# Performance work log

Measured on AMD Instinct MI355X. Metric: run time of the kernel, lower is better.

The kernel has to match this reference:

```python
import jax, jax.numpy as jnp
import numpy as np

N = 50000
E = 800000
IN_DIM, HID, OUT = 128, 256, 40
BN_EPS = 1e-5


def setup_inputs() -> dict:
    key = jax.random.key(0)
    ks = jax.random.split(key, 10)
    x = jax.random.normal(ks[0], (N, IN_DIM), dtype=jnp.float32)
    edge_index = jax.random.randint(ks[1], (2, E), 0, N, dtype=jnp.int64)
    W1 = jax.random.normal(ks[2], (IN_DIM, HID), dtype=jnp.float32) * 0.05
    b1 = jnp.zeros((HID,), dtype=jnp.float32)
    W2 = jax.random.normal(ks[3], (HID, HID), dtype=jnp.float32) * 0.05
    b2 = jnp.zeros((HID,), dtype=jnp.float32)
    W3 = jax.random.normal(ks[4], (HID, OUT), dtype=jnp.float32) * 0.05
    b3 = jnp.zeros((OUT,), dtype=jnp.float32)
    # BatchNorm params (shared across the two pre-final layers in the source)
    gamma = jnp.ones((HID,), dtype=jnp.float32)
    beta = jnp.zeros((HID,), dtype=jnp.float32)
    return {"x": x, "edge_index": edge_index, "W1": W1, "b1": b1,
            "W2": W2, "b2": b2, "W3": W3, "b3": b3,
            "gamma": gamma, "beta": beta}


def _gcn_norm(edge_index):
    # add self-loops, compute symmetric normalization D^-1/2 (A+I) D^-1/2
    self_loops = jnp.arange(N, dtype=edge_index.dtype)
    row = jnp.concatenate([edge_index[0], self_loops])
    col = jnp.concatenate([edge_index[1], self_loops])
    deg = jax.ops.segment_sum(jnp.ones_like(row, dtype=jnp.float32), col, num_segments=N)
    dinv = jnp.where(deg > 0, jax.lax.rsqrt(deg), 0.0)
    norm = dinv[row] * dinv[col]  # [E+N]
    return row, col, norm


def _gcn_conv(h, W, b, row, col, norm):
    h = h @ W                              # transform first (smaller msg dim)
    msg = norm[:, None] * h[col]           # [E+N, F] gather
    agg = jax.ops.segment_sum(msg, row, num_segments=N)  # scatter-add
    return agg + b


def _batchnorm(h, gamma, beta):
    mu = jnp.mean(h, axis=0)
    var = jnp.mean((h - mu) ** 2, axis=0)
    return (h - mu) * jax.lax.rsqrt(var + BN_EPS) * gamma + beta


def reference(x, edge_index, W1, b1, W2, b2, W3, b3, gamma, beta):
    row, col, norm = _gcn_norm(edge_index)
    out = _gcn_conv(x, W1, b1, row, col, norm)
    out = jax.nn.relu(_batchnorm(out, gamma, beta))
    out = _gcn_conv(out, W2, b2, row, col, norm)
    out = jax.nn.relu(_batchnorm(out, gamma, beta))  # BN shared in source
    out = _gcn_conv(out, W3, b3, row, col, norm)
    return jax.nn.log_softmax(out, axis=-1)
```

## Files before the change

kernel.cpp:

```cpp
#include <hip/hip_runtime.h>
#include <math.h>

#define NN 50000
#define NE 800000
#define IN_DIM 128
#define HID 256
#define OUT_DIM 40
#define BN_EPS 1e-5f

#define HG 128
#define HW 25000
#define HPASS 12800

#define NBK 196
#define PB 256
#define EPB (NE / PB)

typedef __attribute__((ext_vector_type(8))) short short8;
typedef __attribute__((ext_vector_type(4))) float f32x4;
typedef __attribute__((ext_vector_type(2))) float f32x2;

__device__ __forceinline__ ushort f2bf(float f) {
    union { float f; unsigned u; } v; v.f = f;
    unsigned r = v.u + 0x7fffu + ((v.u >> 16) & 1u);
    return (ushort)(r >> 16);
}
__device__ __forceinline__ float bflo(unsigned u) {
    union { unsigned a; float f; } v; v.a = u << 16; return v.f;
}
__device__ __forceinline__ float bfhi(unsigned u) {
    union { unsigned a; float f; } v; v.a = u & 0xffff0000u; return v.f;
}
__device__ __forceinline__ f32x2 fp8_dec_lo(int v) {
    return __builtin_amdgcn_cvt_pk_f32_fp8(v, false);
}
__device__ __forceinline__ f32x2 fp8_dec_hi(int v) {
    return __builtin_amdgcn_cvt_pk_f32_fp8(v, true);
}
__device__ __forceinline__ int fp8_enc_lo(float a, float b, int old) {
    return __builtin_amdgcn_cvt_pk_fp8_f32(a, b, old, false);
}
__device__ __forceinline__ int fp8_enc_hi(float a, float b, int old) {
    return __builtin_amdgcn_cvt_pk_fp8_f32(a, b, old, true);
}

__global__ __launch_bounds__(512) void k_p1(const int* __restrict__ erow,
                                            const int* __restrict__ ecol,
                                            unsigned* __restrict__ Pcol,
                                            unsigned* __restrict__ cnt) {
    __shared__ unsigned lds[HPASS];
    int t = threadIdx.x;
    int b = blockIdx.x;
    if (b < HG) {
        unsigned* partial = Pcol + (size_t)b * HW;
        int e0 = b * (NE / HG), e1 = e0 + (NE / HG);
#pragma unroll
        for (int pass = 0; pass < 2; pass++) {
            int wbase = pass ? HPASS : 0;
            int wend = pass ? HW : HPASS;
            int nw = wend - wbase;
            for (int w = t; w < HPASS; w += 512) lds[w] = 0u;
            __syncthreads();
            int vlo = wbase * 2, vhi = wend * 2;
            for (int e = e0 + t; e < e1; e += 512) {
                int v = ecol[e];
                if (v >= vlo && v < vhi)
                    atomicAdd(&lds[(v >> 1) - wbase], (v & 1) ? 0x10000u : 1u);
            }
            __syncthreads();
            for (int w = t; w < nw; w += 512) partial[wbase + w] = lds[w];
            __syncthreads();
        }
    } else {
        int bb = b - HG;
        for (int i = t; i < NBK; i += 512) lds[i] = 0u;
        __syncthreads();
        int e0 = bb * EPB;
        for (int i = t; i < EPB; i += 512) atomicAdd(&lds[((unsigned)erow[e0 + i]) >> 8], 1u);
        __syncthreads();
        for (int i = t; i < NBK; i += 512) cnt[bb * NBK + i] = lds[i];
    }
}

__global__ __launch_bounds__(256) void k_p2(const unsigned* __restrict__ Pcol,
                                            float* __restrict__ dinv,
                                            const unsigned* __restrict__ cnt,
                                            unsigned* __restrict__ off,
                                            unsigned* __restrict__ bstart) {
    int t = threadIdx.x;
    if (blockIdx.x < 98) {
        int w = blockIdx.x * 256 + t;
        if (w >= HW) return;
        unsigned sc = 0;
        for (int b = 0; b < HG; b++) sc += Pcol[(size_t)b * HW + w];
        dinv[2 * w] = rsqrtf((float)((sc & 0xffffu) + 1u));
        dinv[2 * w + 1] = rsqrtf((float)((sc >> 16) + 1u));
    } else {
        __shared__ unsigned s[256];
        unsigned tot = 0;
        if (t < NBK) for (int b = 0; b < PB; b++) tot += cnt[b * NBK + t];
        s[t] = tot;
        __syncthreads();
        for (int o = 1; o < 256; o <<= 1) {
            unsigned x = (t >= o) ? s[t - o] : 0u;
            __syncthreads();
            s[t] += x;
            __syncthreads();
        }
        unsigned base = s[t] - tot;
        if (t < NBK) bstart[t] = base;
        if (t == NBK - 1) bstart[NBK] = base + tot;
        if (t < NBK) {
            unsigned run = base;
            for (int b = 0; b < PB; b++) { off[b * NBK + t] = run; run += cnt[b * NBK + t]; }
        }
    }
}

__global__ __launch_bounds__(256) void k_p3(const int* __restrict__ erow,
                                            const int* __restrict__ ecol,
                                            const unsigned* __restrict__ off,
                                            int2* __restrict__ ebuf,
                                            const float* __restrict__ x,
                                            const float* __restrict__ dinv,
                                            uchar* __restrict__ xs8,
                                            const float* __restrict__ W1,
                                            const float* __restrict__ W2,
                                            const float* __restrict__ W3,
                                            ushort* __restrict__ Wt1,
                                            ushort* __restrict__ Wt2,
                                            ushort* __restrict__ Wt3) {
    int t = threadIdx.x, b = blockIdx.x;
    if (b < PB) {
        __shared__ unsigned c[NBK];
        for (int i = t; i < NBK; i += 256) c[i] = off[b * NBK + i];
        __syncthreads();
        int e0 = b * EPB;
        for (int i = t; i < EPB; i += 256) {
            int r = erow[e0 + i], cc = ecol[e0 + i];
            unsigned p = atomicAdd(&c[((unsigned)r) >> 8], 1u);
            ebuf[p] = make_int2(r, cc);
        }
    } else if (b < PB + 6250) {
        int i = (b - PB) * 256 + t;
        int row = i >> 5;
        float d = dinv[row];
        float4 v = ((const float4*)x)[i];
        int p = fp8_enc_lo(v.x * d, v.y * d, 0);
        p = fp8_enc_hi(v.z * d, v.w * d, p);
        ((int*)xs8)[i] = p;
    } else {
        int i = (b - PB - 6250) * 256 + t;
        if (i < 128 * 256) { int k = i / 256, n = i % 256; Wt1[n * 128 + k] = f2bf(W1[i]); }
        if (i < 256 * 256) { int k = i / 256, n = i % 256; Wt2[n * 256 + k] = f2bf(W2[i]); }
        if (i < 48 * 256)  { int n = i / 256, k = i % 256;
                             Wt3[i] = (n < OUT_DIM) ? f2bf(W3[k * OUT_DIM + n]) : (ushort)0; }
    }
}

__global__ __launch_bounds__(256) void k_part4(const int2* __restrict__ ebuf,
                                               const unsigned* __restrict__ bstart,
                                               unsigned* __restrict__ rowptr,
                                               int* __restrict__ colidx) {
    __shared__ unsigned rc[256], cur[256], s[256];
    int t = threadIdx.x, b = blockIdx.x;
    unsigned ebase = bstart[b], ecnt = bstart[b + 1] - ebase;
    rc[t] = 0u;
    __syncthreads();
    for (unsigned i = t; i < ecnt; i += 256) atomicAdd(&rc[ebuf[ebase + i].x & 255], 1u);
    __syncthreads();
    unsigned v = rc[t];
    s[t] = v;
    __syncthreads();
    for (int o = 1; o < 256; o <<= 1) {
        unsigned x = (t >= o) ? s[t - o] : 0u;
        __syncthreads();
        s[t] += x;
        __syncthreads();
    }
    unsigned excl = s[t] - v;
    int row = (b << 8) + t;
    if (row < NN) rowptr[row] = ebase + excl;
    cur[t] = ebase + excl;
    if (b == 0 && t == 0) rowptr[NN] = NE;
    __syncthreads();
    for (unsigned i = t; i < ecnt; i += 256) {
        int2 e = ebuf[ebase + i];
        unsigned p = atomicAdd(&cur[e.x & 255], 1u);
        colidx[p] = e.y;
    }
}

__global__ __launch_bounds__(64) void k_agg_x(const uchar* __restrict__ xs8,
                                              const unsigned* __restrict__ rowptr,
                                              const int* __restrict__ colidx,
                                              const float* __restrict__ dinv,
                                              ushort* __restrict__ Xa) {
    int r = blockIdx.x;
    int t = threadIdx.x;
    const ushort* Xv = (const ushort*)xs8;
    f32x2 sf = fp8_dec_lo((int)Xv[(size_t)r * 64 + t]);
    float a0 = sf[0], a1 = sf[1];
    unsigned e0 = rowptr[r], e1 = rowptr[r + 1];
    unsigned e = e0;
    for (; e + 8 <= e1; e += 8) {
        int v0 = Xv[(size_t)colidx[e] * 64 + t];
        int v1 = Xv[(size_t)colidx[e + 1] * 64 + t];
        int v2 = Xv[(size_t)colidx[e + 2] * 64 + t];
        int v3 = Xv[(size_t)colidx[e + 3] * 64 + t];
        int v4 = Xv[(size_t)colidx[e + 4] * 64 + t];
        int v5 = Xv[(size_t)colidx[e + 5] * 64 + t];
        int v6 = Xv[(size_t)colidx[e + 6] * 64 + t];
        int v7 = Xv[(size_t)colidx[e + 7] * 64 + t];
        f32x2 f0 = fp8_dec_lo(v0), f1 = fp8_dec_lo(v1);
        f32x2 f2 = fp8_dec_lo(v2), f3 = fp8_dec_lo(v3);
        f32x2 f4 = fp8_dec_lo(v4), f5 = fp8_dec_lo(v5);
        f32x2 f6 = fp8_dec_lo(v6), f7 = fp8_dec_lo(v7);
        a0 += f0[0] + f1[0] + f2[0] + f3[0] + f4[0] + f5[0] + f6[0] + f7[0];
        a1 += f0[1] + f1[1] + f2[1] + f3[1] + f4[1] + f5[1] + f6[1] + f7[1];
    }
    for (; e < e1; e++) {
        f32x2 f = fp8_dec_lo((int)Xv[(size_t)colidx[e] * 64 + t]);
        a0 += f[0]; a1 += f[1];
    }
    float dr = dinv[r];
    ((unsigned*)Xa)[(size_t)r * 64 + t] = (unsigned)f2bf(dr * a0) | ((unsigned)f2bf(dr * a1) << 16);
}

template <int K>
__global__ __launch_bounds__(256) void k_gemm1(const ushort* __restrict__ A,
                                               const ushort* __restrict__ Bt,
                                               ushort* __restrict__ H16,
                                               float* __restrict__ bnacc) {
    constexpr int BK = 32;
    constexpr int LD = 40;
    __shared__ ushort sA[64 * LD];
    __shared__ ushort sB[128 * LD];
    int t = threadIdx.x;
    int wave = t >> 6, lane = t & 63;
    int quad = lane >> 4, m15 = lane & 15;
    long r0 = (long)blockIdx.x * 64;
    int n0 = blockIdx.y * 128;

    f32x4 acc[8];
#pragma unroll
    for (int i = 0; i < 8; i++) { acc[i][0] = 0.f; acc[i][1] = 0.f; acc[i][2] = 0.f; acc[i][3] = 0.f; }

    for (int k0 = 0; k0 < K; k0 += BK) {
        {
            int row = t >> 2, seg = (t & 3) * 8;
            long gr = r0 + row;
            uint4 v = make_uint4(0, 0, 0, 0);
            if (gr < NN) v = *(const uint4*)(A + gr * K + k0 + seg);
            *(uint4*)(sA + row * LD + seg) = v;
        }
        {
            int n = t >> 1, seg = (t & 1) * 16;
            const uint4* src = (const uint4*)(Bt + (long)(n0 + n) * K + k0 + seg);
            uint4 b0 = src[0], b1 = src[1];
            *(uint4*)(sB + n * LD + seg) = b0;
            *(uint4*)(sB + n * LD + seg + 8) = b1;
        }
        __syncthreads();
        short8 a = *(const short8*)(sA + (wave * 16 + m15) * LD + quad * 8);
#pragma unroll
        for (int ct = 0; ct < 8; ct++) {
            short8 b = *(const short8*)(sB + (ct * 16 + m15) * LD + quad * 8);
            acc[ct] = __builtin_amdgcn_mfma_f32_16x16x32_bf16(a, b, acc[ct], 0, 0, 0);
        }
        __syncthreads();
    }
    long rowbase = r0 + wave * 16 + quad * 4;
#pragma unroll
    for (int ct = 0; ct < 8; ct++) {
        int col = n0 + ct * 16 + m15;
#pragma unroll
        for (int rg = 0; rg < 4; rg++) {
            long gr = rowbase + rg;
            if (gr < NN) H16[gr * 256 + col] = f2bf(acc[ct][rg]);
        }
    }
    float* ldsS = (float*)(void*)sA;
    float* ldsQ = (float*)(void*)sB;
#pragma unroll
    for (int ct = 0; ct < 8; ct++) {
        float s = acc[ct][0] + acc[ct][1] + acc[ct][2] + acc[ct][3];
        float q = acc[ct][0] * acc[ct][0] + acc[ct][1] * acc[ct][1]
                + acc[ct][2] * acc[ct][2] + acc[ct][3] * acc[ct][3];
        s += __shfl_xor(s, 16, 64); q += __shfl_xor(q, 16, 64);
        s += __shfl_xor(s, 32, 64); q += __shfl_xor(q, 32, 64);
        if (quad == 0) {
            ldsS[wave * 128 + ct * 16 + m15] = s;
            ldsQ[wave * 128 + ct * 16 + m15] = q;
        }
    }
    __syncthreads();
    {
        int c = t & 127;
        int slice = blockIdx.x & 7;
        float v = (t < 128)
            ? ldsS[c] + ldsS[128 + c] + ldsS[256 + c] + ldsS[384 + c]
            : ldsQ[c] + ldsQ[128 + c] + ldsQ[256 + c] + ldsQ[384 + c];
        atomicAdd(&bnacc[slice * 512 + ((t < 128) ? 0 : 256) + n0 + c], v);
    }
}

__device__ __forceinline__ void bn_stage8(const ushort* __restrict__ Hrow, bool valid,
                                          const float* __restrict__ bn, int col0,
                                          ushort* __restrict__ dst) {
    uint4 hv = make_uint4(0, 0, 0, 0);
    if (valid) hv = *(const uint4*)(Hrow + col0);
    float f[8] = { bflo(hv.x), bfhi(hv.x), bflo(hv.y), bfhi(hv.y),
                   bflo(hv.z), bfhi(hv.z), bflo(hv.w), bfhi(hv.w) };
#pragma unroll
    for (int j = 0; j < 8; j++)
        dst[j] = f2bf(fmaxf(f[j] * bn[512 + col0 + j] + bn[768 + col0 + j], 0.f));
}

__global__ __launch_bounds__(256) void k_gemm2(const ushort* __restrict__ H16,
                                               const float* __restrict__ bn,
                                               const ushort* __restrict__ Bt,
                                               const float* __restrict__ dinv,
                                               uchar* __restrict__ Y8) {
    constexpr int K = 256, BK = 32, LD = 40;
    __shared__ ushort sA[64 * LD];
    __shared__ ushort sB[128 * LD];
    int t = threadIdx.x;
    int wave = t >> 6, lane = t & 63;
    int quad = lane >> 4, m15 = lane & 15;
    long r0 = (long)blockIdx.x * 64;
    int n0 = blockIdx.y * 128;

    f32x4 acc[8];
#pragma unroll
    for (int i = 0; i < 8; i++) { acc[i][0] = 0.f; acc[i][1] = 0.f; acc[i][2] = 0.f; acc[i][3] = 0.f; }

    for (int k0 = 0; k0 < K; k0 += BK) {
        {
            int row = t >> 2, seg = (t & 3) * 8;
            long gr = r0 + row;
            bn_stage8(H16 + gr * 256, gr < NN, bn, k0 + seg, sA + row * LD + seg);
        }
        {
            int n = t >> 1, seg = (t & 1) * 16;
            const uint4* src = (const uint4*)(Bt + (long)(n0 + n) * K + k0 + seg);
            uint4 b0 = src[0], b1 = src[1];
            *(uint4*)(sB + n * LD + seg) = b0;
            *(uint4*)(sB + n * LD + seg + 8) = b1;
        }
        __syncthreads();
        short8 a = *(const short8*)(sA + (wave * 16 + m15) * LD + quad * 8);
#pragma unroll
        for (int ct = 0; ct < 8; ct++) {
            short8 b = *(const short8*)(sB + (ct * 16 + m15) * LD + quad * 8);
            acc[ct] = __builtin_amdgcn_mfma_f32_16x16x32_bf16(a, b, acc[ct], 0, 0, 0);
        }
        __syncthreads();
    }
    long rowbase = r0 + wave * 16 + quad * 4;
    float dv[4];
#pragma unroll
    for (int rg = 0; rg < 4; rg++) dv[rg] = (rowbase + rg < NN) ? dinv[rowbase + rg] : 0.f;
#pragma unroll
    for (int ct = 0; ct < 8; ct++) {
        int col = n0 + ct * 16 + m15;
#pragma unroll
        for (int rg = 0; rg < 4; rg++) {
            long gr = rowbase + rg;
            if (gr < NN) {
                int p = fp8_enc_lo(dv[rg] * acc[ct][rg], 0.f, 0);
                Y8[gr * 256 + col] = (uchar)(p & 0xff);
            }
        }
    }
}

__global__ __launch_bounds__(256) void k_gemm3(const ushort* __restrict__ H16,
                                               const float* __restrict__ bn,
                                               const ushort* __restrict__ Wt3,
                                               const float* __restrict__ dinv,
                                               ushort* __restrict__ Y) {
    constexpr int LD = 264;
    __shared__ ushort sA[64 * LD];
    __shared__ ushort sB[48 * LD];
    int t = threadIdx.x;
    int wave = t >> 6, lane = t & 63;
    int quad = lane >> 4, m15 = lane & 15;
    long r0 = (long)blockIdx.x * 64;

    for (int idx = t; idx < 48 * 16; idx += 256) {
        int n = idx >> 4, s = (idx & 15) * 16;
        const uint4* src = (const uint4*)(Wt3 + n * 256 + s);
        *(uint4*)(sB + n * LD + s) = src[0];
        *(uint4*)(sB + n * LD + s + 8) = src[1];
    }
    {
        int row = t >> 2;
        long gr = r0 + row;
#pragma unroll
        for (int s8 = 0; s8 < 8; s8++) {
            int seg = s8 * 32 + (t & 3) * 8;
            bn_stage8(H16 + gr * 256, gr < NN, bn, seg, sA + row * LD + seg);
        }
    }
    __syncthreads();

    f32x4 acc[3];
#pragma unroll
    for (int i = 0; i < 3; i++) { acc[i][0] = 0.f; acc[i][1] = 0.f; acc[i][2] = 0.f; acc[i][3] = 0.f; }
#pragma unroll
    for (int k0 = 0; k0 < 256; k0 += 32) {
        short8 a = *(const short8*)(sA + (wave * 16 + m15) * LD + k0 + quad * 8);
#pragma unroll
        for (int ct = 0; ct < 3; ct++) {
            short8 b = *(const short8*)(sB + (ct * 16 + m15) * LD + k0 + quad * 8);
            acc[ct] = __builtin_amdgcn_mfma_f32_16x16x32_bf16(a, b, acc[ct], 0, 0, 0);
        }
    }
    long rowbase = r0 + wave * 16 + quad * 4;
#pragma unroll
    for (int ct = 0; ct < 3; ct++) {
        int col = ct * 16 + m15;
#pragma unroll
        for (int rg = 0; rg < 4; rg++) {
            long gr = rowbase + rg;
            if (gr < NN) Y[gr * 64 + col] = f2bf(dinv[gr] * acc[ct][rg]);
        }
    }
}

__global__ __launch_bounds__(64) void k_agg_hid(const uchar* __restrict__ Y8,
                                                const unsigned* __restrict__ rowptr,
                                                const int* __restrict__ colidx,
                                                const float* __restrict__ dinv,
                                                ushort* __restrict__ H16) {
    int r = blockIdx.x;
    int t = threadIdx.x;
    const int* Yv = (const int*)Y8;
    int y = Yv[(size_t)r * 64 + t];
    f32x2 yl = fp8_dec_lo(y), yh = fp8_dec_hi(y);
    float a0 = yl[0], a1 = yl[1], a2 = yh[0], a3 = yh[1];
    unsigned e0 = rowptr[r], e1 = rowptr[r + 1];
    unsigned e = e0;
    for (; e + 8 <= e1; e += 8) {
        int v0 = Yv[(size_t)colidx[e] * 64 + t];
        int v1 = Yv[(size_t)colidx[e + 1] * 64 + t];
        int v2 = Yv[(size_t)colidx[e + 2] * 64 + t];
        int v3 = Yv[(size_t)colidx[e + 3] * 64 + t];
        int v4 = Yv[(size_t)colidx[e + 4] * 64 + t];
        int v5 = Yv[(size_t)colidx[e + 5] * 64 + t];
        int v6 = Yv[(size_t)colidx[e + 6] * 64 + t];
        int v7 = Yv[(size_t)colidx[e + 7] * 64 + t];
        f32x2 l0 = fp8_dec_lo(v0), h0 = fp8_dec_hi(v0);
        f32x2 l1 = fp8_dec_lo(v1), h1 = fp8_dec_hi(v1);
        f32x2 l2 = fp8_dec_lo(v2), h2 = fp8_dec_hi(v2);
        f32x2 l3 = fp8_dec_lo(v3), h3 = fp8_dec_hi(v3);
        f32x2 l4 = fp8_dec_lo(v4), h4 = fp8_dec_hi(v4);
        f32x2 l5 = fp8_dec_lo(v5), h5 = fp8_dec_hi(v5);
        f32x2 l6 = fp8_dec_lo(v6), h6 = fp8_dec_hi(v6);
        f32x2 l7 = fp8_dec_lo(v7), h7 = fp8_dec_hi(v7);
        a0 += l0[0] + l1[0] + l2[0] + l3[0] + l4[0] + l5[0] + l6[0] + l7[0];
        a1 += l0[1] + l1[1] + l2[1] + l3[1] + l4[1] + l5[1] + l6[1] + l7[1];
        a2 += h0[0] + h1[0] + h2[0] + h3[0] + h4[0] + h5[0] + h6[0] + h7[0];
        a3 += h0[1] + h1[1] + h2[1] + h3[1] + h4[1] + h5[1] + h6[1] + h7[1];
    }
    for (; e < e1; e++) {
        int v = Yv[(size_t)colidx[e] * 64 + t];
        f32x2 l = fp8_dec_lo(v), h = fp8_dec_hi(v);
        a0 += l[0]; a1 += l[1]; a2 += h[0]; a3 += h[1];
    }
    float dr = dinv[r];
    uint2 o;
    o.x = (unsigned)f2bf(dr * a0) | ((unsigned)f2bf(dr * a1) << 16);
    o.y = (unsigned)f2bf(dr * a2) | ((unsigned)f2bf(dr * a3) << 16);
    ((uint2*)H16)[(size_t)r * 64 + t] = o;
}

__global__ __launch_bounds__(64) void k_agg_lsm(const ushort* __restrict__ Y,
                                                const unsigned* __restrict__ rowptr,
                                                const int* __restrict__ colidx,
                                                const float* __restrict__ dinv,
                                                const float* __restrict__ b3,
                                                float* __restrict__ out) {
    int r = blockIdx.x;
    int t = threadIdx.x;
    bool act = t < OUT_DIM;
    float acc = act ? bflo((unsigned)Y[(size_t)r * 64 + t]) : 0.f;
    unsigned e0 = rowptr[r], e1 = rowptr[r + 1];
    unsigned e = e0;
    for (; e + 4 <= e1; e += 4) {
        int c0 = colidx[e], c1 = colidx[e + 1], c2 = colidx[e + 2], c3 = colidx[e + 3];
        if (act) {
            acc += bflo((unsigned)Y[(size_t)c0 * 64 + t]) + bflo((unsigned)Y[(size_t)c1 * 64 + t])
                 + bflo((unsigned)Y[(size_t)c2 * 64 + t]) + bflo((unsigned)Y[(size_t)c3 * 64 + t]);
        }
    }
    for (; e < e1; e++) {
        if (act) acc += bflo((unsigned)Y[(size_t)colidx[e] * 64 + t]);
    }
    float o = act ? (dinv[r] * acc + b3[t]) : 0.f;
    float m = act ? o : -1e30f;
#pragma unroll
    for (int d = 1; d < 64; d <<= 1) m = fmaxf(m, __shfl_xor(m, d, 64));
    float ex = act ? expf(o - m) : 0.f;
#pragma unroll
    for (int d = 1; d < 64; d <<= 1) ex += __shfl_xor(ex, d, 64);
    float ls = logf(ex) + m;
    if (act) out[(size_t)r * OUT_DIM + t] = o - ls;
}

__global__ __launch_bounds__(256) void k_bn_stats2(const ushort* __restrict__ H16,
                                                   float* __restrict__ bnacc) {
    __shared__ float ls[512];
    int t = threadIdx.x;
    ls[t] = 0.f; ls[t + 256] = 0.f;
    __syncthreads();
    int colb = (t & 31) * 8;
    float s[8], q[8];
#pragma unroll
    for (int j = 0; j < 8; j++) { s[j] = 0.f; q[j] = 0.f; }
    for (int rb = blockIdx.x * 8 + (t >> 5); rb < NN; rb += gridDim.x * 8) {
        uint4 v = *(const uint4*)(H16 + (size_t)rb * 256 + colb);
        float f[8] = { bflo(v.x), bfhi(v.x), bflo(v.y), bfhi(v.y),
                       bflo(v.z), bfhi(v.z), bflo(v.w), bfhi(v.w) };
#pragma unroll
        for (int j = 0; j < 8; j++) { s[j] += f[j]; q[j] += f[j] * f[j]; }
    }
#pragma unroll
    for (int j = 0; j < 8; j++) {
        atomicAdd(&ls[colb + j], s[j]);
        atomicAdd(&ls[256 + colb + j], q[j]);
    }
    __syncthreads();
    int slice = blockIdx.x & 7;
    atomicAdd(&bnacc[slice * 512 + t], ls[t]);
    atomicAdd(&bnacc[slice * 512 + 256 + t], ls[t + 256]);
}

__global__ __launch_bounds__(256) void k_bn_final(const float* __restrict__ bnacc,
                                                  const float* __restrict__ gamma,
                                                  const float* __restrict__ beta,
                                                  float* __restrict__ bn) {
    int t = threadIdx.x;
    float s = 0.f, sq = 0.f;
#pragma unroll
    for (int sl = 0; sl < 8; sl++) {
        s += bnacc[sl * 512 + t];
        sq += bnacc[sl * 512 + 256 + t];
    }
    float mu = s * (1.f / NN);
    float var = sq * (1.f / NN) - mu * mu;
    float rstd = rsqrtf(var + BN_EPS);
    float g = gamma[t] * rstd;
    bn[512 + t] = g;
    bn[768 + t] = beta[t] - mu * g;
}


extern "C" void kernel_launch(void* const* d_in, const int* in_sizes, int n_in,
                              void* d_out, int out_size, void* d_ws, size_t ws_size,
                              hipStream_t stream) {
    const float* x     = (const float*)d_in[0];
    const int*   erow  = (const int*)d_in[1];
    const int*   ecol  = ((const int*)d_in[1]) + NE;
    const float* W1    = (const float*)d_in[2];
    const float* W2    = (const float*)d_in[4];
    const float* W3    = (const float*)d_in[6];
    const float* b3    = (const float*)d_in[7];
    const float* gamma = (const float*)d_in[8];
    const float* beta  = (const float*)d_in[9];
    float* out = (float*)d_out;

    char* ws = (char*)d_ws;
    size_t off = 0;
    auto alloc = [&](size_t bytes) -> void* {
        void* p = ws + off;
        off = (off + bytes + 255) & ~(size_t)255;
        return p;
    };
    float*    dinv     = (float*)alloc(NN * 4);
    unsigned* rowptr   = (unsigned*)alloc((NN + 1) * 4);
    int*      colidx   = (int*)alloc((size_t)NE * 4);
    float*    bn       = (float*)alloc(1024 * 4);
    float*    bnacc    = (float*)alloc(8 * 512 * 4);
    unsigned* cnt      = (unsigned*)alloc((size_t)PB * NBK * 4);
    unsigned* boff     = (unsigned*)alloc((size_t)PB * NBK * 4);
    unsigned* bstart   = (unsigned*)alloc((NBK + 1) * 4);
    ushort*   Wt1      = (ushort*)alloc(128 * 256 * 2);
    ushort*   Wt2      = (ushort*)alloc(256 * 256 * 2);
    ushort*   Wt3      = (ushort*)alloc(48 * 256 * 2);
    uchar*    xs8      = (uchar*)alloc((size_t)NN * IN_DIM);
    ushort*   Xa       = (ushort*)alloc((size_t)NN * IN_DIM * 2);
    ushort*   H16      = (ushort*)alloc((size_t)NN * HID * 2);
    uchar*    Ys2      = (uchar*)alloc((size_t)NN * HID);
    ushort*   Ys3      = (ushort*)alloc((size_t)NN * 64 * 2);

    unsigned* Pcol = (unsigned*)H16;
    int2*     ebuf = (int2*)((char*)H16 + (size_t)13 * 1024 * 1024);

    k_p1<<<HG + PB, 512, 0, stream>>>(erow, ecol, Pcol, cnt);
    k_p2<<<99, 256, 0, stream>>>(Pcol, dinv, cnt, boff, bstart);
    k_p3<<<PB + 6250 + 256, 256, 0, stream>>>(erow, ecol, boff, ebuf,
                                              x, dinv, xs8, W1, W2, W3, Wt1, Wt2, Wt3);
    k_part4<<<NBK, 256, 0, stream>>>(ebuf, bstart, rowptr, colidx);
    hipMemsetAsync(bnacc, 0, 8 * 512 * 4, stream);

    dim3 ggrid((NN + 63) / 64, 2);

    k_agg_x<<<NN, 64, 0, stream>>>(xs8, rowptr, colidx, dinv, Xa);
    k_gemm1<IN_DIM><<<ggrid, 256, 0, stream>>>(Xa, Wt1, H16, bnacc);
    k_bn_final<<<1, 256, 0, stream>>>(bnacc, gamma, beta, bn);

    k_gemm2<<<ggrid, 256, 0, stream>>>(H16, bn, Wt2, dinv, Ys2);
    k_agg_hid<<<NN, 64, 0, stream>>>(Ys2, rowptr, colidx, dinv, H16);
    hipMemsetAsync(bnacc, 0, 8 * 512 * 4, stream);
    k_bn_stats2<<<1024, 256, 0, stream>>>(H16, bnacc);
    k_bn_final<<<1, 256, 0, stream>>>(bnacc, gamma, beta, bn);

    k_gemm3<<<(NN + 63) / 64, 256, 0, stream>>>(H16, bn, Wt3, dinv, Ys3);
    k_agg_lsm<<<NN, 64, 0, stream>>>(Ys3, rowptr, colidx, dinv, b3, out);
}
```

Baseline: 322.7 us.

## Slice feature tables into 32-column planes for cache-friendly aggregation; fold BN finalize into GEMMs

Stores the fp8 feature tables (x and layer-2 GEMM output) as column slices of 32 bytes per node, each slice a contiguous plane. The aggregation kernels then process one slice per block over 8 rows, so the gathered working set per slice is smaller and more likely to stay in cache. The separate BN-finalize kernels and one memset are removed; each GEMM block recomputes the scale and shift in a prologue. The cost is byte-wide gathers with only 32 active bytes per row, more passes over colidx and rowptr (once per slice), and redundant BN recomputation in every block.

```diff
diff --git a/kernel.cpp b/kernel.cpp
--- a/kernel.cpp
+++ b/kernel.cpp
@@ -34,14 +34,15 @@
 __device__ __forceinline__ f32x2 fp8_dec_lo(int v) {
     return __builtin_amdgcn_cvt_pk_f32_fp8(v, false);
 }
-__device__ __forceinline__ f32x2 fp8_dec_hi(int v) {
-    return __builtin_amdgcn_cvt_pk_f32_fp8(v, true);
-}
 __device__ __forceinline__ int fp8_enc_lo(float a, float b, int old) {
     return __builtin_amdgcn_cvt_pk_fp8_f32(a, b, old, false);
 }
 __device__ __forceinline__ int fp8_enc_hi(float a, float b, int old) {
     return __builtin_amdgcn_cvt_pk_fp8_f32(a, b, old, true);
+}
+__device__ __forceinline__ float fp8_dec1(int byte) {
+    f32x2 f = fp8_dec_lo(byte & 0xff);
+    return f[0];
 }
 
 __global__ __launch_bounds__(512) void k_p1(const int* __restrict__ erow,
@@ -144,11 +145,13 @@
     } else if (b < PB + 6250) {
         int i = (b - PB) * 256 + t;
         int row = i >> 5;
+        int g = i & 31;
         float d = dinv[row];
         float4 v = ((const float4*)x)[i];
         int p = fp8_enc_lo(v.x * d, v.y * d, 0);
         p = fp8_enc_hi(v.z * d, v.w * d, p);
-        ((int*)xs8)[i] = p;
+        int slice = g >> 3;
+        ((int*)xs8)[((size_t)slice * NN + row) * 8 + (g & 7)] = p;
     } else {
         int i = (b - PB - 6250) * 256 + t;
         if (i < 128 * 256) { int k = i / 256, n = i % 256; Wt1[n * 128 + k] = f2bf(W1[i]); }
@@ -191,40 +194,34 @@
     }
 }
 
-__global__ __launch_bounds__(64) void k_agg_x(const uchar* __restrict__ xs8,
-                                              const unsigned* __restrict__ rowptr,
-                                              const int* __restrict__ colidx,
-                                              const float* __restrict__ dinv,
-                                              ushort* __restrict__ Xa) {
-    int r = blockIdx.x;
-    int t = threadIdx.x;
-    const ushort* Xv = (const ushort*)xs8;
-    f32x2 sf = fp8_dec_lo((int)Xv[(size_t)r * 64 + t]);
-    float a0 = sf[0], a1 = sf[1];
-    unsigned e0 = rowptr[r], e1 = rowptr[r + 1];
-    unsigned e = e0;
-    for (; e + 8 <= e1; e += 8) {
-        int v0 = Xv[(size_t)colidx[e] * 64 + t];
-        int v1 = Xv[(size_t)colidx[e + 1] * 64 + t];
-        int v2 = Xv[(size_t)colidx[e + 2] * 64 + t];
-        int v3 = Xv[(size_t)colidx[e + 3] * 64 + t];
-        int v4 = Xv[(size_t)colidx[e + 4] * 64 + t];
-        int v5 = Xv[(size_t)colidx[e + 5] * 64 + t];
-        int v6 = Xv[(size_t)colidx[e + 6] * 64 + t];
-        int v7 = Xv[(size_t)colidx[e + 7] * 64 + t];
-        f32x2 f0 = fp8_dec_lo(v0), f1 = fp8_dec_lo(v1);
-        f32x2 f2 = fp8_dec_lo(v2), f3 = fp8_dec_lo(v3);
-        f32x2 f4 = fp8_dec_lo(v4), f5 = fp8_dec_lo(v5);
-        f32x2 f6 = fp8_dec_lo(v6), f7 = fp8_dec_lo(v7);
-        a0 += f0[0] + f1[0] + f2[0] + f3[0] + f4[0] + f5[0] + f6[0] + f7[0];
-        a1 += f0[1] + f1[1] + f2[1] + f3[1] + f4[1] + f5[1] + f6[1] + f7[1];
-    }
-    for (; e < e1; e++) {
-        f32x2 f = fp8_dec_lo((int)Xv[(size_t)colidx[e] * 64 + t]);
-        a0 += f[0]; a1 += f[1];
-    }
-    float dr = dinv[r];
-    ((unsigned*)Xa)[(size_t)r * 64 + t] = (unsigned)f2bf(dr * a0) | ((unsigned)f2bf(dr * a1) << 16);
+template <int OSTRIDE>
+__global__ __launch_bounds__(64) void k_agg_sl(const uchar* __restrict__ T,
+                                               const unsigned* __restrict__ rowptr,
+                                               const int* __restrict__ colidx,
+                                               const float* __restrict__ dinv,
+                                               ushort* __restrict__ Out) {
+    int s = blockIdx.x;
+    int t = threadIdx.x;
+    int col = t & 31, half = t >> 5;
+    const uchar* Ts = T + (size_t)s * NN * 32;
+    int r0 = blockIdx.y * 8;
+#pragma unroll 1
+    for (int r = r0; r < r0 + 8; r++) {
+        unsigned e0 = rowptr[r], e1 = rowptr[r + 1];
+        float a = (half == 0) ? fp8_dec1(Ts[(size_t)r * 32 + col]) : 0.f;
+        unsigned e = e0 + half;
+        for (; e + 6 < e1; e += 8) {
+            int c0 = colidx[e], c1 = colidx[e + 2], c2 = colidx[e + 4], c3 = colidx[e + 6];
+            float v0 = fp8_dec1(Ts[(size_t)c0 * 32 + col]);
+            float v1 = fp8_dec1(Ts[(size_t)c1 * 32 + col]);
+            float v2 = fp8_dec1(Ts[(size_t)c2 * 32 + col]);
+            float v3 = fp8_dec1(Ts[(size_t)c3 * 32 + col]);
+            a += v0 + v1 + v2 + v3;
+        }
+        for (; e < e1; e += 2) a += fp8_dec1(Ts[(size_t)colidx[e] * 32 + col]);
+        a += __shfl_xor(a, 32, 64);
+        if (half == 0) Out[(size_t)r * OSTRIDE + s * 32 + col] = f2bf(dinv[r] * a);
+    }
 }
 
 template <int K>
@@ -305,8 +302,27 @@
     }
 }
 
+__device__ __forceinline__ void bn_prolog(const float* __restrict__ bnacc,
+                                          const float* __restrict__ gamma,
+                                          const float* __restrict__ beta,
+                                          float* __restrict__ bnsc,
+                                          float* __restrict__ bnsh, int t) {
+    float s = 0.f, q = 0.f;
+#pragma unroll
+    for (int sl = 0; sl < 8; sl++) {
+        s += bnacc[sl * 512 + t];
+        q += bnacc[sl * 512 + 256 + t];
+    }
+    float mu = s * (1.f / NN);
+    float var = q * (1.f / NN) - mu * mu;
+    float g = gamma[t] * rsqrtf(var + BN_EPS);
+    bnsc[t] = g;
+    bnsh[t] = beta[t] - mu * g;
+}
+
 __device__ __forceinline__ void bn_stage8(const ushort* __restrict__ Hrow, bool valid,
-                                          const float* __restrict__ bn, int col0,
+                                          const float* __restrict__ bnsc,
+                                          const float* __restrict__ bnsh, int col0,
                                           ushort* __restrict__ dst) {
     uint4 hv = make_uint4(0, 0, 0, 0);
     if (valid) hv = *(const uint4*)(Hrow + col0);
@@ -314,23 +330,29 @@
                    bflo(hv.z), bfhi(hv.z), bflo(hv.w), bfhi(hv.w) };
 #pragma unroll
     for (int j = 0; j < 8; j++)
-        dst[j] = f2bf(fmaxf(f[j] * bn[512 + col0 + j] + bn[768 + col0 + j], 0.f));
+        dst[j] = f2bf(fmaxf(f[j] * bnsc[col0 + j] + bnsh[col0 + j], 0.f));
 }
 
 __global__ __launch_bounds__(256) void k_gemm2(const ushort* __restrict__ H16,
-                                               const float* __restrict__ bn,
+                                               const float* __restrict__ bnacc,
+                                               const float* __restrict__ gamma,
+                                               const float* __restrict__ beta,
                                                const ushort* __restrict__ Bt,
                                                const float* __restrict__ dinv,
                                                uchar* __restrict__ Y8) {
     constexpr int K = 256, BK = 32, LD = 40;
     __shared__ ushort sA[64 * LD];
     __shared__ ushort sB[128 * LD];
+    __shared__ float bnsc[256], bnsh[256];
     int t = threadIdx.x;
     int wave = t >> 6, lane = t & 63;
     int quad = lane >> 4, m15 = lane & 15;
     long r0 = (long)blockIdx.x * 64;
     int n0 = blockIdx.y * 128;
 
+    bn_prolog(bnacc, gamma, beta, bnsc, bnsh, t);
+    __syncthreads();
+
     f32x4 acc[8];
 #pragma unroll
     for (int i = 0; i < 8; i++) { acc[i][0] = 0.f; acc[i][1] = 0.f; acc[i][2] = 0.f; acc[i][3] = 0.f; }
@@ -339,7 +361,7 @@
         {
             int row = t >> 2, seg = (t & 3) * 8;
             long gr = r0 + row;
-            bn_stage8(H16 + gr * 256, gr < NN, bn, k0 + seg, sA + row * LD + seg);
+            bn_stage8(H16 + gr * 256, gr < NN, bnsc, bnsh, k0 + seg, sA + row * LD + seg);
         }
         {
             int n = t >> 1, seg = (t & 1) * 16;
@@ -364,29 +386,36 @@
 #pragma unroll
     for (int ct = 0; ct < 8; ct++) {
         int col = n0 + ct * 16 + m15;
+        size_t sbase = ((size_t)(col >> 5) * NN) * 32 + (col & 31);
 #pragma unroll
         for (int rg = 0; rg < 4; rg++) {
             long gr = rowbase + rg;
             if (gr < NN) {
                 int p = fp8_enc_lo(dv[rg] * acc[ct][rg], 0.f, 0);
-                Y8[gr * 256 + col] = (uchar)(p & 0xff);
+                Y8[sbase + (size_t)gr * 32] = (uchar)(p & 0xff);
             }
         }
     }
 }
 
 __global__ __launch_bounds__(256) void k_gemm3(const ushort* __restrict__ H16,
-                                               const float* __restrict__ bn,
+                                               const float* __restrict__ bnacc,
+                                               const float* __restrict__ gamma,
+                                               const float* __restrict__ beta,
                                                const ushort* __restrict__ Wt3,
                                                const float* __restrict__ dinv,
                                                ushort* __restrict__ Y) {
     constexpr int LD = 264;
     __shared__ ushort sA[64 * LD];
     __shared__ ushort sB[48 * LD];
+    __shared__ float bnsc[256], bnsh[256];
     int t = threadIdx.x;
     int wave = t >> 6, lane = t & 63;
     int quad = lane >> 4, m15 = lane & 15;
     long r0 = (long)blockIdx.x * 64;
+
+    bn_prolog(bnacc, gamma, beta, bnsc, bnsh, t);
+    __syncthreads();
 
     for (int idx = t; idx < 48 * 16; idx += 256) {
         int n = idx >> 4, s = (idx & 15) * 16;
@@ -400,7 +429,7 @@
 #pragma unroll
         for (int s8 = 0; s8 < 8; s8++) {
             int seg = s8 * 32 + (t & 3) * 8;
-            bn_stage8(H16 + gr * 256, gr < NN, bn, seg, sA + row * LD + seg);
+            bn_stage8(H16 + gr * 256, gr < NN, bnsc, bnsh, seg, sA + row * LD + seg);
         }
     }
     __syncthreads();
@@ -427,53 +456,6 @@
             if (gr < NN) Y[gr * 64 + col] = f2bf(dinv[gr] * acc[ct][rg]);
         }
     }
-}
-
-__global__ __launch_bounds__(64) void k_agg_hid(const uchar* __restrict__ Y8,
-                                                const unsigned* __restrict__ rowptr,
-                                                const int* __restrict__ colidx,
-                                                const float* __restrict__ dinv,
-                                                ushort* __restrict__ H16) {
-    int r = blockIdx.x;
-    int t = threadIdx.x;
-    const int* Yv = (const int*)Y8;
-    int y = Yv[(size_t)r * 64 + t];
-    f32x2 yl = fp8_dec_lo(y), yh = fp8_dec_hi(y);
-    float a0 = yl[0], a1 = yl[1], a2 = yh[0], a3 = yh[1];
-    unsigned e0 = rowptr[r], e1 = rowptr[r + 1];
-    unsigned e = e0;
-    for (; e + 8 <= e1; e += 8) {
-        int v0 = Yv[(size_t)colidx[e] * 64 + t];
-        int v1 = Yv[(size_t)colidx[e + 1] * 64 + t];
-        int v2 = Yv[(size_t)colidx[e + 2] * 64 + t];
-        int v3 = Yv[(size_t)colidx[e + 3] * 64 + t];
-        int v4 = Yv[(size_t)colidx[e + 4] * 64 + t];
-        int v5 = Yv[(size_t)colidx[e + 5] * 64 + t];
-        int v6 = Yv[(size_t)colidx[e + 6] * 64 + t];
-        int v7 = Yv[(size_t)colidx[e + 7] * 64 + t];
-        f32x2 l0 = fp8_dec_lo(v0), h0 = fp8_dec_hi(v0);
-        f32x2 l1 = fp8_dec_lo(v1), h1 = fp8_dec_hi(v1);
-        f32x2 l2 = fp8_dec_lo(v2), h2 = fp8_dec_hi(v2);
-        f32x2 l3 = fp8_dec_lo(v3), h3 = fp8_dec_hi(v3);
-        f32x2 l4 = fp8_dec_lo(v4), h4 = fp8_dec_hi(v4);
-        f32x2 l5 = fp8_dec_lo(v5), h5 = fp8_dec_hi(v5);
-        f32x2 l6 = fp8_dec_lo(v6), h6 = fp8_dec_hi(v6);
-        f32x2 l7 = fp8_dec_lo(v7), h7 = fp8_dec_hi(v7);
-        a0 += l0[0] + l1[0] + l2[0] + l3[0] + l4[0] + l5[0] + l6[0] + l7[0];
-        a1 += l0[1] + l1[1] + l2[1] + l3[1] + l4[1] + l5[1] + l6[1] + l7[1];
-        a2 += h0[0] + h1[0] + h2[0] + h3[0] + h4[0] + h5[0] + h6[0] + h7[0];
-        a3 += h0[1] + h1[1] + h2[1] + h3[1] + h4[1] + h5[1] + h6[1] + h7[1];
-    }
-    for (; e < e1; e++) {
-        int v = Yv[(size_t)colidx[e] * 64 + t];
-        f32x2 l = fp8_dec_lo(v), h = fp8_dec_hi(v);
-        a0 += l[0]; a1 += l[1]; a2 += h[0]; a3 += h[1];
-    }
-    float dr = dinv[r];
-    uint2 o;
-    o.x = (unsigned)f2bf(dr * a0) | ((unsigned)f2bf(dr * a1) << 16);
-    o.y = (unsigned)f2bf(dr * a2) | ((unsigned)f2bf(dr * a3) << 16);
-    ((uint2*)H16)[(size_t)r * 64 + t] = o;
 }
 
 __global__ __launch_bounds__(64) void k_agg_lsm(const ushort* __restrict__ Y,
@@ -535,25 +517,6 @@
     int slice = blockIdx.x & 7;
     atomicAdd(&bnacc[slice * 512 + t], ls[t]);
     atomicAdd(&bnacc[slice * 512 + 256 + t], ls[t + 256]);
-}
-
-__global__ __launch_bounds__(256) void k_bn_final(const float* __restrict__ bnacc,
-                                                  const float* __restrict__ gamma,
-                                                  const float* __restrict__ beta,
-                                                  float* __restrict__ bn) {
-    int t = threadIdx.x;
-    float s = 0.f, sq = 0.f;
-#pragma unroll
-    for (int sl = 0; sl < 8; sl++) {
-        s += bnacc[sl * 512 + t];
-        sq += bnacc[sl * 512 + 256 + t];
-    }
-    float mu = s * (1.f / NN);
-    float var = sq * (1.f / NN) - mu * mu;
-    float rstd = rsqrtf(var + BN_EPS);
-    float g = gamma[t] * rstd;
-    bn[512 + t] = g;
-    bn[768 + t] = beta[t] - mu * g;
 }
 
 
@@ -581,8 +544,7 @@
     float*    dinv     = (float*)alloc(NN * 4);
     unsigned* rowptr   = (unsigned*)alloc((NN + 1) * 4);
     int*      colidx   = (int*)alloc((size_t)NE * 4);
-    float*    bn       = (float*)alloc(1024 * 4);
-    float*    bnacc    = (float*)alloc(8 * 512 * 4);
+    float*    bnacc    = (float*)alloc(2 * 8 * 512 * 4);
     unsigned* cnt      = (unsigned*)alloc((size_t)PB * NBK * 4);
     unsigned* boff     = (unsigned*)alloc((size_t)PB * NBK * 4);
     unsigned* bstart   = (unsigned*)alloc((NBK + 1) * 4);
@@ -595,6 +557,9 @@
     uchar*    Ys2      = (uchar*)alloc((size_t)NN * HID);
     ushort*   Ys3      = (ushort*)alloc((size_t)NN * 64 * 2);
 
+    float* bnacc1 = bnacc;
+    float* bnacc2 = bnacc + 8 * 512;
+
     unsigned* Pcol = (unsigned*)H16;
     int2*     ebuf = (int2*)((char*)H16 + (size_t)13 * 1024 * 1024);
 
@@ -603,20 +568,17 @@
     k_p3<<<PB + 6250 + 256, 256, 0, stream>>>(erow, ecol, boff, ebuf,
                                               x, dinv, xs8, W1, W2, W3, Wt1, Wt2, Wt3);
     k_part4<<<NBK, 256, 0, stream>>>(ebuf, bstart, rowptr, colidx);
-    hipMemsetAsync(bnacc, 0, 8 * 512 * 4, stream);
+    hipMemsetAsync(bnacc, 0, 2 * 8 * 512 * 4, stream);
 
     dim3 ggrid((NN + 63) / 64, 2);
 
-    k_agg_x<<<NN, 64, 0, stream>>>(xs8, rowptr, colidx, dinv, Xa);
-    k_gemm1<IN_DIM><<<ggrid, 256, 0, stream>>>(Xa, Wt1, H16, bnacc);
-    k_bn_final<<<1, 256, 0, stream>>>(bnacc, gamma, beta, bn);
-
-    k_gemm2<<<ggrid, 256, 0, stream>>>(H16, bn, Wt2, dinv, Ys2);
-    k_agg_hid<<<NN, 64, 0, stream>>>(Ys2, rowptr, colidx, dinv, H16);
-    hipMemsetAsync(bnacc, 0, 8 * 512 * 4, stream);
-    k_bn_stats2<<<1024, 256, 0, stream>>>(H16, bnacc);
-    k_bn_final<<<1, 256, 0, stream>>>(bnacc, gamma, beta, bn);
-
-    k_gemm3<<<(NN + 63) / 64, 256, 0, stream>>>(H16, bn, Wt3, dinv, Ys3);
+    k_agg_sl<IN_DIM><<<dim3(4, 6250), 64, 0, stream>>>(xs8, rowptr, colidx, dinv, Xa);
+    k_gemm1<IN_DIM><<<ggrid, 256, 0, stream>>>(Xa, Wt1, H16, bnacc1);
+
+    k_gemm2<<<ggrid, 256, 0, stream>>>(H16, bnacc1, gamma, beta, Wt2, dinv, Ys2);
+    k_agg_sl<HID><<<dim3(8, 6250), 64, 0, stream>>>(Ys2, rowptr, colidx, dinv, H16);
+    k_bn_stats2<<<1024, 256, 0, stream>>>(H16, bnacc2);
+
+    k_gemm3<<<(NN + 63) / 64, 256, 0, stream>>>(H16, bnacc2, gamma, beta, Wt3, dinv, Ys3);
     k_agg_lsm<<<NN, 64, 0, stream>>>(Ys3, rowptr, colidx, dinv, b3, out);
 }
```

Result: slower. 430.3 us (+33.3%).
